# Kernel tuning notes

Measured on AMD Instinct MI355X. Metric: run time of the kernel, lower is better.

## Reference

```python
import jax, jax.numpy as jnp
import numpy as np


def _dct_basis(N):
    # X[k] = 2 * sum_n x[n] * cos(pi * k * (2n+1) / (2N))  -- matches the
    # flip+concat+rfft+twiddle path of the torch module (unnormalized DCT-II x2).
    k = jnp.arange(N, dtype=jnp.float32)[:, None]
    n = jnp.arange(N, dtype=jnp.float32)[None, :]
    return 2.0 * jnp.cos(jnp.pi * k * (2.0 * n + 1.0) / (2.0 * N))  # (K, N)


def _dct2(x):
    B, C, H, W = x.shape
    Bw = _dct_basis(W)
    Bh = _dct_basis(H)
    x = jnp.einsum('bchw,kw->bchk', x, Bw)  # DCT along W
    x = jnp.einsum('bchw,kh->bckw', x, Bh)  # DCT along H
    return x


def _conv3x3(x, w, b):
    y = jax.lax.conv_general_dilated(x, w, window_strides=(1, 1), padding='SAME',
                                     dimension_numbers=('NCHW', 'OIHW', 'NCHW'))
    return y + b[None, :, None, None]


def _bn(x, g, be, m, v):
    # inference-mode BatchNorm2d, eps = 1e-5
    inv = jax.lax.rsqrt(v + 1e-5)
    return (x - m[None, :, None, None]) * (g * inv)[None, :, None, None] + be[None, :, None, None]


def setup_inputs() -> dict:
    key = jax.random.key(0)
    ks = jax.random.split(key, 16)
    B, C, H, W = 32, 1, 224, 224
    mid, emb = 128, 256
    s = 0.05
    return {
        'x':  jax.random.normal(ks[0], (B, C, H, W), jnp.float32),
        'w1': jax.random.normal(ks[1], (64, C, 3, 3), jnp.float32) * s,
        'b1': jax.random.normal(ks[2], (64,), jnp.float32) * s,
        'g1': jax.random.uniform(ks[3], (64,), jnp.float32, 0.5, 1.5),
        'be1': jax.random.normal(ks[4], (64,), jnp.float32) * s,
        'm1': jax.random.normal(ks[5], (64,), jnp.float32) * s,
        'v1': jax.random.uniform(ks[6], (64,), jnp.float32, 0.5, 1.5),
        'w2': jax.random.normal(ks[7], (mid, 64, 3, 3), jnp.float32) * s,
        'b2': jax.random.normal(ks[8], (mid,), jnp.float32) * s,
        'g2': jax.random.uniform(ks[9], (mid,), jnp.float32, 0.5, 1.5),
        'be2': jax.random.normal(ks[10], (mid,), jnp.float32) * s,
        'm2': jax.random.normal(ks[11], (mid,), jnp.float32) * s,
        'v2': jax.random.uniform(ks[12], (mid,), jnp.float32, 0.5, 1.5),
        'wp': jax.random.normal(ks[13], (emb, mid), jnp.float32) * s,
        'bp': jax.random.normal(ks[14], (emb,), jnp.float32) * s,
    }


def reference(x, w1, b1, g1, be1, m1, v1, w2, b2, g2, be2, m2, v2, wp, bp):
    USE_TOPK = 0.5
    X = _dct2(x)                                   # (B, 1, H, W)
    B, C, H, W = X.shape
    k_h, k_w = int(H * USE_TOPK), int(W * USE_TOPK)
    mask = jnp.zeros((H, W), X.dtype).at[:k_h, :k_w].set(1.0)
    X = X * mask[None, None]
    h = jax.nn.relu(_bn(_conv3x3(X, w1, b1), g1, be1, m1, v1))
    h = jax.nn.relu(_bn(_conv3x3(h, w2, b2), g2, be2, m2, v2))
    h = jnp.mean(h, axis=(2, 3))                   # AdaptiveAvgPool2d((1,1)) -> (B, mid)
    return h @ wp.T + bp                           # (B, emb_dim)
```

## Files before the change

kernel.cpp:

```cpp
#include <hip/hip_runtime.h>
#include <math.h>


#define NPIX 224
#define KEEP 112
#define H1DIM 115
#define NPX1 (H1DIM * H1DIM)
#define ADIM 114

typedef short bf16x8 __attribute__((ext_vector_type(8)));
typedef float f32x16 __attribute__((ext_vector_type(16)));

__device__ __forceinline__ unsigned short f2bf(float f) {
    unsigned int u = __float_as_uint(f);
    unsigned int r = (u + 0x7FFFu + ((u >> 16) & 1u)) >> 16;
    return (unsigned short)r;
}

__global__ __launch_bounds__(256) void prep_kernel(
    const float* __restrict__ w1, const float* __restrict__ b1,
    const float* __restrict__ g1, const float* __restrict__ be1,
    const float* __restrict__ m1, const float* __restrict__ v1,
    const float* __restrict__ w2,
    float* __restrict__ Bst, float* __restrict__ P,
    float* __restrict__ ws1, float* __restrict__ wb1,
    uint4* __restrict__ w2f) {
    int bp = blockIdx.x, tid = threadIdx.x;
    if (bp < 49) {
        int idx = bp * 256 + tid;
        if (idx < KEEP * KEEP) {
            int n = idx / KEEP, k = idx - n * KEEP;
            double ang = 3.14159265358979323846 * (double)k * (2.0 * n + 1.0) / (2.0 * NPIX);
            Bst[n * KEEP + k] = (float)(2.0 * cos(ang));
        }
    } else if (bp < 54) {
        __shared__ float c1s[64];
        if (tid < 64) {
            float sc = g1[tid] * rsqrtf(v1[tid] + 1e-5f);
            c1s[tid] = fmaxf((b1[tid] - m1[tid]) * sc + be1[tid], 0.f);
        }
        __syncthreads();
        int idx = (bp - 49) * 256 + tid;
        if (idx < 128 * 9) {
            int oc = idx / 9, tap = idx - oc * 9;
            float s = 0.f;
            for (int ic = 0; ic < 64; ++ic)
                s = fmaf(w2[((size_t)oc * 64 + ic) * 9 + tap], c1s[ic], s);
            P[idx] = s;
        }
    } else if (bp == 54) {
        if (tid < 64) {
            float sc = g1[tid] * rsqrtf(v1[tid] + 1e-5f);
            wb1[tid] = (b1[tid] - m1[tid]) * sc + be1[tid];
            for (int t = 0; t < 9; ++t) ws1[tid * 9 + t] = w1[tid * 9 + t] * sc;
        }
    } else {
        int j = (bp - 55) * 256 + tid;
        if (j < 9216) {
            int q = j >> 6, lane = j & 63;
            int tap = q / 16, rem = q & 15;
            int kc = rem >> 2, g32 = rem & 3;
            int oc = g32 * 32 + (lane & 31);
            int ic0 = kc * 16 + (lane >> 5) * 8;
            union { unsigned short us[8]; uint4 v; } u;
#pragma unroll
            for (int t_ = 0; t_ < 8; ++t_)
                u.us[t_] = f2bf(w2[((size_t)oc * 64 + ic0 + t_) * 9 + tap]);
            w2f[j] = u.v;
        }
    }
}

__global__ __launch_bounds__(256) void dct_w_kernel(const float* __restrict__ x,
                                                    const float* __restrict__ Bst,
                                                    float* __restrict__ tmp1) {
    int bx = blockIdx.x, tid = threadIdx.x;
    __shared__ float eo[2][8][112];
    const float* rows = x + (size_t)bx * 8 * NPIX;
    for (int i = tid; i < 896; i += 256) {
        int r = i / 112, n = i - r * 112;
        float a = rows[r * NPIX + n], bv = rows[r * NPIX + 223 - n];
        eo[0][r][n] = a + bv;
        eo[1][r][n] = a - bv;
    }
    __syncthreads();
    int kw = tid & 127, rh = tid >> 7;
    if (kw >= KEEP) return;
    const float* eop = &eo[kw & 1][rh * 4][0];
    float a0 = 0.f, a1 = 0.f, a2 = 0.f, a3 = 0.f;
    for (int n = 0; n < 112; ++n) {
        float bs = Bst[n * KEEP + kw];
        a0 = fmaf(eop[n], bs, a0);
        a1 = fmaf(eop[112 + n], bs, a1);
        a2 = fmaf(eop[224 + n], bs, a2);
        a3 = fmaf(eop[336 + n], bs, a3);
    }
    size_t base = ((size_t)bx * 8 + rh * 4) * KEEP + kw;
    tmp1[base] = a0; tmp1[base + 112] = a1; tmp1[base + 224] = a2; tmp1[base + 336] = a3;
}

__global__ __launch_bounds__(512) void dct_h_kernel(const float* __restrict__ tmp1,
                                                    const float* __restrict__ Bst,
                                                    float* __restrict__ Xd) {
    int kq = blockIdx.x, b = blockIdx.y;
    int tid = threadIdx.x;
    int kw = tid & 127, sub = tid >> 7;
    __shared__ float ps[3][4][112];
    const int kh0 = kq * 4;
    float a0 = 0.f, a1 = 0.f, a2 = 0.f, a3 = 0.f;
    if (kw < KEEP) {
        const float* t = tmp1 + (size_t)b * NPIX * KEEP + kw;
        for (int h = sub * 28; h < sub * 28 + 28; ++h) {
            float lo = t[(size_t)h * KEEP];
            float hi = t[(size_t)(223 - h) * KEEP];
            float e = lo + hi, o = lo - hi;
            const float* bs = Bst + h * KEEP + kh0;
            a0 = fmaf(e, bs[0], a0);
            a1 = fmaf(o, bs[1], a1);
            a2 = fmaf(e, bs[2], a2);
            a3 = fmaf(o, bs[3], a3);
        }
        if (sub) {
            ps[sub - 1][0][kw] = a0; ps[sub - 1][1][kw] = a1;
            ps[sub - 1][2][kw] = a2; ps[sub - 1][3][kw] = a3;
        }
    }
    __syncthreads();
    if (sub == 0 && kw < KEEP) {
        a0 += ps[0][0][kw] + ps[1][0][kw] + ps[2][0][kw];
        a1 += ps[0][1][kw] + ps[1][1][kw] + ps[2][1][kw];
        a2 += ps[0][2][kw] + ps[1][2][kw] + ps[2][2][kw];
        a3 += ps[0][3][kw] + ps[1][3][kw] + ps[2][3][kw];
        float* X = Xd + ((size_t)b * KEEP + kh0) * KEEP + kw;
        X[0] = a0; X[112] = a1; X[224] = a2; X[336] = a3;
    }
}

__global__ __launch_bounds__(256) void conv1_kernel(const float* __restrict__ Xd,
                                                    const float* __restrict__ ws1,
                                                    const float* __restrict__ wb1,
                                                    unsigned short* __restrict__ h1c) {
    const int b = blockIdx.y;
    const int p0 = blockIdx.x * 256;
    const int tid = threadIdx.x;
    const int p = p0 + tid;
    __shared__ uint4 Lt[2048];

    const bool valid = p < NPX1;
    int r = p / H1DIM, c = p - r * H1DIM;
    const float* X = Xd + (size_t)b * KEEP * KEEP;
    float xv[9];
#pragma unroll
    for (int ky = 0; ky < 3; ++ky)
#pragma unroll
        for (int kx = 0; kx < 3; ++kx) {
            int rr = r + ky - 1, cc = c + kx - 1;
            xv[ky * 3 + kx] =
                (valid && (unsigned)rr < (unsigned)KEEP && (unsigned)cc < (unsigned)KEEP)
                    ? X[rr * KEEP + cc] : 0.f;
        }

#pragma unroll 1
    for (int icg = 0; icg < 8; ++icg) {
        union { unsigned short us[8]; uint4 v; } u;
#pragma unroll
        for (int j = 0; j < 8; ++j) {
            int ic = icg * 8 + j;
            float s = wb1[ic];
#pragma unroll
            for (int t = 0; t < 9; ++t) s = fmaf(xv[t], ws1[ic * 9 + t], s);
            u.us[j] = f2bf(fmaxf(s, 0.f));
        }
        Lt[tid * 8 + (icg ^ (tid & 7))] = u.v;
    }
    __syncthreads();

#pragma unroll
    for (int k = 0; k < 8; ++k) {
        int q = k * 256 + tid;
        int pxl = q >> 3, ig = q & 7;
        uint4 v = Lt[pxl * 8 + (ig ^ (pxl & 7))];
        int pg = p0 + pxl;
        if (pg < NPX1)
            *reinterpret_cast<uint4*>(h1c + ((size_t)b * NPX1 + pg) * 64 + ig * 8) = v;
    }
}

__global__ __launch_bounds__(512, 4) void conv2_mfma_kernel(
    const unsigned short* __restrict__ h1c, const uint4* __restrict__ w2f,
    const float* __restrict__ b2, const float* __restrict__ g2,
    const float* __restrict__ be2, const float* __restrict__ m2,
    const float* __restrict__ v2, float* __restrict__ partial) {
    const int tc = blockIdx.x, tr = blockIdx.y, b = blockIdx.z;
    const int r0 = tr * 16, c0 = tc * 16;
    const int tid = threadIdx.x;
    const int lane = tid & 63, w = tid >> 6;
    const int mg = w & 3, og = w >> 2;

    __shared__ unsigned short At[324 * 64];

    const unsigned short* __restrict__ h1b = h1c + (size_t)b * (NPX1 * 64);
    char* Atw = reinterpret_cast<char*>(At);
    for (int e = tid; e < 2592; e += 512) {
        int px = e >> 3, gi = e & 7;
        int pr = px / 18, pc = px - pr * 18;
        int gr = r0 + pr - 1, gc = c0 + pc - 1;
        uint4 v = make_uint4(0u, 0u, 0u, 0u);
        if ((unsigned)gr < (unsigned)H1DIM && (unsigned)gc < (unsigned)H1DIM)
            v = *reinterpret_cast<const uint4*>(h1b + ((size_t)(gr * H1DIM + gc)) * 64 + gi * 8);
        int off = px * 128 + 32 * ((gi >> 1) ^ (px & 3)) + 16 * ((gi & 1) ^ ((px >> 2) & 1));
        *reinterpret_cast<uint4*>(Atw + off) = v;
    }
    __syncthreads();

    f32x16 acc[2][2];
#pragma unroll
    for (int F = 0; F < 2; ++F)
#pragma unroll
        for (int N = 0; N < 2; ++N)
#pragma unroll
            for (int i = 0; i < 16; ++i) acc[F][N][i] = 0.f;

    const int flim2 = ADIM - r0 - 4 * mg;
    int A0[9];
    {
        const int prb = 4 * mg + ((lane & 31) >> 4);
        const int cb = lane & 15;
        const int hb = lane >> 5;
#pragma unroll
        for (int ky = 0; ky < 3; ++ky)
#pragma unroll
            for (int kx = 0; kx < 3; ++kx) {
                int px = (prb + ky) * 18 + cb + kx;
                A0[ky * 3 + kx] = px * 128 + 32 * (px & 3) + 16 * (hb ^ ((px >> 2) & 1));
            }
    }
    const char* Atc = reinterpret_cast<const char*>(At);

    if (flim2 >= 4) {
#pragma unroll
        for (int s = 0; s < 36; ++s) {
            const int tap = s >> 2, kc = s & 3;
            const int ky = tap / 3, kx = tap - 3 * ky;
            const bf16x8* bq = reinterpret_cast<const bf16x8*>(
                w2f + (size_t)(((tap * 4 + kc) * 4) + og * 2) * 64 + lane);
            const bf16x8 b0 = bq[0];
            const bf16x8 b1 = bq[64];
            const int a0 = A0[ky * 3 + kx] ^ (kc << 5);
            const int a1 = (a0 ^ 16) + 4608;
            const bf16x8 va0 = *reinterpret_cast<const bf16x8*>(Atc + a0);
            const bf16x8 va1 = *reinterpret_cast<const bf16x8*>(Atc + a1);
            acc[0][0] = __builtin_amdgcn_mfma_f32_32x32x16_bf16(va0, b0, acc[0][0], 0, 0, 0);
            acc[0][1] = __builtin_amdgcn_mfma_f32_32x32x16_bf16(va0, b1, acc[0][1], 0, 0, 0);
            acc[1][0] = __builtin_amdgcn_mfma_f32_32x32x16_bf16(va1, b0, acc[1][0], 0, 0, 0);
            acc[1][1] = __builtin_amdgcn_mfma_f32_32x32x16_bf16(va1, b1, acc[1][1], 0, 0, 0);
        }
    } else if (flim2 > 0) {
#pragma unroll
        for (int s = 0; s < 36; ++s) {
            const int tap = s >> 2, kc = s & 3;
            const int ky = tap / 3, kx = tap - 3 * ky;
            const bf16x8* bq = reinterpret_cast<const bf16x8*>(
                w2f + (size_t)(((tap * 4 + kc) * 4) + og * 2) * 64 + lane);
            const bf16x8 b0 = bq[0];
            const bf16x8 b1 = bq[64];
            const int a0 = A0[ky * 3 + kx] ^ (kc << 5);
            const bf16x8 va0 = *reinterpret_cast<const bf16x8*>(Atc + a0);
            acc[0][0] = __builtin_amdgcn_mfma_f32_32x32x16_bf16(va0, b0, acc[0][0], 0, 0, 0);
            acc[0][1] = __builtin_amdgcn_mfma_f32_32x32x16_bf16(va0, b1, acc[0][1], 0, 0, 0);
        }
    }

    const int tile = tr * 8 + tc;
    float* pslice = partial + (((size_t)b * 64 + tile) * 4 + mg) * 128;
#pragma unroll
    for (int N = 0; N < 2; ++N) {
        int oc = og * 64 + N * 32 + (lane & 31);
        float sc = g2[oc] * rsqrtf(v2[oc] + 1e-5f);
        float bias = b2[oc] - m2[oc];
        float add = be2[oc];
        float s = 0.f;
#pragma unroll
        for (int F = 0; F < 2; ++F) {
#pragma unroll
            for (int rg = 0; rg < 16; ++rg) {
                int m = (rg & 3) + 8 * (rg >> 2) + 4 * (lane >> 5);
                int p = ((2 * mg + F) << 5) + m;
                int row = r0 + (p >> 4);
                int col = c0 + (p & 15);
                float v = fmaxf(fmaf(acc[F][N][rg] + bias, sc, add), 0.f);
                s += (row < ADIM && col < ADIM) ? v : 0.f;
            }
        }
        s += __shfl_xor(s, 32);
        if (lane < 32) pslice[og * 64 + N * 32 + lane] = s;
    }
}

__global__ __launch_bounds__(256) void tail_kernel(
    const float* __restrict__ partial, const float* __restrict__ P,
    const float* __restrict__ b2, const float* __restrict__ g2,
    const float* __restrict__ be2, const float* __restrict__ m2,
    const float* __restrict__ v2,
    const float* __restrict__ wp, const float* __restrict__ bp,
    float* __restrict__ out) {
    int b = blockIdx.x, tid = threadIdx.x;
    __shared__ float red[2][128];
    __shared__ float mrow[128];
    int oc = tid & 127, half = tid >> 7;
    const float* pb = partial + (size_t)b * 256 * 128 + oc;
    float s = 0.f;
#pragma unroll 8
    for (int j = 0; j < 128; ++j) s += pb[(size_t)(half * 128 + j) * 128];
    red[half][oc] = s;
    __syncthreads();
    if (tid < 128) {
        float tot = red[0][tid] + red[1][tid];
        float p[9];
#pragma unroll
        for (int t = 0; t < 9; ++t) p[t] = P[tid * 9 + t];
        float Sall = p[0] + p[1] + p[2] + p[3] + p[4] + p[5] + p[6] + p[7] + p[8];
        float Stop = p[3] + p[4] + p[5] + p[6] + p[7] + p[8];
        float Sbot = p[0] + p[1] + p[2] + p[3] + p[4] + p[5];
        float Sleft  = p[1] + p[2] + p[4] + p[5] + p[7] + p[8];
        float Sright = p[0] + p[1] + p[3] + p[4] + p[6] + p[7];
        float Ctr = p[3] + p[4] + p[6] + p[7];
        float Cbl = p[1] + p[2] + p[4] + p[5];
        float Cbr = p[0] + p[1] + p[3] + p[4];
        float bias = b2[tid], mm = m2[tid], bb = be2[tid];
        float sc = g2[tid] * rsqrtf(v2[tid] + 1e-5f);
#define VALOF(S) fmaxf(((bias) + (S) - (mm)) * (sc) + (bb), 0.f)
        float cs = 36515.f * VALOF(Sall) + 109.f * VALOF(Stop) + 109.f * VALOF(Sleft)
                 + 222.f * VALOF(Sbot) + 222.f * VALOF(Sright)
                 + VALOF(Ctr) + VALOF(Cbl) + VALOF(Cbr);
#undef VALOF
        mrow[tid] = (tot + cs) * (1.f / (224.f * 224.f));
    }
    __syncthreads();
    const float4* wr = reinterpret_cast<const float4*>(wp + (size_t)tid * 128);
    float acc = bp[tid];
#pragma unroll 8
    for (int c = 0; c < 32; ++c) {
        float4 wv = wr[c];
        acc = fmaf(mrow[4 * c], wv.x, acc);
        acc = fmaf(mrow[4 * c + 1], wv.y, acc);
        acc = fmaf(mrow[4 * c + 2], wv.z, acc);
        acc = fmaf(mrow[4 * c + 3], wv.w, acc);
    }
    out[(size_t)b * 256 + tid] = acc;
}

extern "C" void kernel_launch(void* const* d_in, const int* in_sizes, int n_in,
                              void* d_out, int out_size, void* d_ws, size_t ws_size,
                              hipStream_t stream) {
    const float* x   = (const float*)d_in[0];
    const float* w1  = (const float*)d_in[1];
    const float* b1  = (const float*)d_in[2];
    const float* g1  = (const float*)d_in[3];
    const float* be1 = (const float*)d_in[4];
    const float* m1  = (const float*)d_in[5];
    const float* v1  = (const float*)d_in[6];
    const float* w2  = (const float*)d_in[7];
    const float* b2  = (const float*)d_in[8];
    const float* g2  = (const float*)d_in[9];
    const float* be2 = (const float*)d_in[10];
    const float* m2  = (const float*)d_in[11];
    const float* v2  = (const float*)d_in[12];
    const float* wp  = (const float*)d_in[13];
    const float* bp  = (const float*)d_in[14];
    float* out = (float*)d_out;

    float* ws = (float*)d_ws;
    size_t off = 0;
    float* Bst  = ws + off; off += (size_t)KEEP * KEEP;
    float* tmp1 = ws + off; off += (size_t)32 * NPIX * KEEP;
    float* Xd   = ws + off; off += (size_t)32 * KEEP * KEEP;
    float* P    = ws + off; off += 128 * 9;
    float* ws1  = ws + off; off += 64 * 9;
    float* wb1  = ws + off; off += 64;
    uint4* w2f  = (uint4*)(ws + off); off += (size_t)9216 * 4;
    float* part = ws + off; off += (size_t)32 * 256 * 128;
    unsigned short* h1c = (unsigned short*)(ws + off);
    off += (size_t)32 * NPX1 * 64 / 2;

    if (ws_size < off * sizeof(float)) return;

    prep_kernel<<<dim3(91), dim3(256), 0, stream>>>(w1, b1, g1, be1, m1, v1, w2,
                                                    Bst, P, ws1, wb1, w2f);
    dct_w_kernel<<<dim3(896), dim3(256), 0, stream>>>(x, Bst, tmp1);
    dct_h_kernel<<<dim3(28, 32), dim3(512), 0, stream>>>(tmp1, Bst, Xd);
    conv1_kernel<<<dim3(52, 32), dim3(256), 0, stream>>>(Xd, ws1, wb1, h1c);
    conv2_mfma_kernel<<<dim3(8, 8, 32), dim3(512), 0, stream>>>(
        h1c, w2f, b2, g2, be2, m2, v2, part);
    tail_kernel<<<dim3(32), dim3(256), 0, stream>>>(part, P, b2, g2, be2, m2, v2, wp, bp, out);
}
```

Measured before the change: 127.3 us.

## Fuse conv1 into conv2 tile load, recomputing halo in shared memory

Removes the separate conv1 kernel and its bf16 h1 intermediate buffer in global memory. Each conv2 block now loads a 20x20 patch of the masked DCT output into shared memory and computes the 18x18x64 conv1+BN+ReLU halo tile directly into the swizzled LDS layout. This eliminates the write and reread of roughly 54 MB of activations and one launch. In exchange, the halo pixels are computed redundantly, and the per-block prologue is heavier, which may lengthen conv2's critical path.

```diff
diff --git a/kernel.cpp b/kernel.cpp
--- a/kernel.cpp
+++ b/kernel.cpp
@@ -5,7 +5,6 @@
 #define NPIX 224
 #define KEEP 112
 #define H1DIM 115
-#define NPX1 (H1DIM * H1DIM)
 #define ADIM 114
 
 typedef short bf16x8 __attribute__((ext_vector_type(8)));
@@ -136,58 +135,9 @@
     }
 }
 
-__global__ __launch_bounds__(256) void conv1_kernel(const float* __restrict__ Xd,
-                                                    const float* __restrict__ ws1,
-                                                    const float* __restrict__ wb1,
-                                                    unsigned short* __restrict__ h1c) {
-    const int b = blockIdx.y;
-    const int p0 = blockIdx.x * 256;
-    const int tid = threadIdx.x;
-    const int p = p0 + tid;
-    __shared__ uint4 Lt[2048];
-
-    const bool valid = p < NPX1;
-    int r = p / H1DIM, c = p - r * H1DIM;
-    const float* X = Xd + (size_t)b * KEEP * KEEP;
-    float xv[9];
-#pragma unroll
-    for (int ky = 0; ky < 3; ++ky)
-#pragma unroll
-        for (int kx = 0; kx < 3; ++kx) {
-            int rr = r + ky - 1, cc = c + kx - 1;
-            xv[ky * 3 + kx] =
-                (valid && (unsigned)rr < (unsigned)KEEP && (unsigned)cc < (unsigned)KEEP)
-                    ? X[rr * KEEP + cc] : 0.f;
-        }
-
-#pragma unroll 1
-    for (int icg = 0; icg < 8; ++icg) {
-        union { unsigned short us[8]; uint4 v; } u;
-#pragma unroll
-        for (int j = 0; j < 8; ++j) {
-            int ic = icg * 8 + j;
-            float s = wb1[ic];
-#pragma unroll
-            for (int t = 0; t < 9; ++t) s = fmaf(xv[t], ws1[ic * 9 + t], s);
-            u.us[j] = f2bf(fmaxf(s, 0.f));
-        }
-        Lt[tid * 8 + (icg ^ (tid & 7))] = u.v;
-    }
-    __syncthreads();
-
-#pragma unroll
-    for (int k = 0; k < 8; ++k) {
-        int q = k * 256 + tid;
-        int pxl = q >> 3, ig = q & 7;
-        uint4 v = Lt[pxl * 8 + (ig ^ (pxl & 7))];
-        int pg = p0 + pxl;
-        if (pg < NPX1)
-            *reinterpret_cast<uint4*>(h1c + ((size_t)b * NPX1 + pg) * 64 + ig * 8) = v;
-    }
-}
-
-__global__ __launch_bounds__(512, 4) void conv2_mfma_kernel(
-    const unsigned short* __restrict__ h1c, const uint4* __restrict__ w2f,
+__global__ __launch_bounds__(512, 4) void conv2_fused_kernel(
+    const float* __restrict__ Xd, const float* __restrict__ ws1,
+    const float* __restrict__ wb1, const uint4* __restrict__ w2f,
     const float* __restrict__ b2, const float* __restrict__ g2,
     const float* __restrict__ be2, const float* __restrict__ m2,
     const float* __restrict__ v2, float* __restrict__ partial) {
@@ -198,18 +148,43 @@
     const int mg = w & 3, og = w >> 2;
 
     __shared__ unsigned short At[324 * 64];
-
-    const unsigned short* __restrict__ h1b = h1c + (size_t)b * (NPX1 * 64);
+    __shared__ float Xs[20][21];
+    __shared__ float wbs[64];
+
+    const float* __restrict__ Xb = Xd + (size_t)b * KEEP * KEEP;
+    for (int i = tid; i < 400; i += 512) {
+        int rr = i / 20, cc = i - rr * 20;
+        int gr = r0 - 2 + rr, gc = c0 - 2 + cc;
+        Xs[rr][cc] = ((unsigned)gr < (unsigned)KEEP && (unsigned)gc < (unsigned)KEEP)
+                         ? Xb[gr * KEEP + gc] : 0.f;
+    }
+    if (tid < 64) wbs[tid] = wb1[tid];
+    __syncthreads();
+
     char* Atw = reinterpret_cast<char*>(At);
     for (int e = tid; e < 2592; e += 512) {
-        int px = e >> 3, gi = e & 7;
+        int px = e >> 3, icg = e & 7;
         int pr = px / 18, pc = px - pr * 18;
         int gr = r0 + pr - 1, gc = c0 + pc - 1;
-        uint4 v = make_uint4(0u, 0u, 0u, 0u);
-        if ((unsigned)gr < (unsigned)H1DIM && (unsigned)gc < (unsigned)H1DIM)
-            v = *reinterpret_cast<const uint4*>(h1b + ((size_t)(gr * H1DIM + gc)) * 64 + gi * 8);
-        int off = px * 128 + 32 * ((gi >> 1) ^ (px & 3)) + 16 * ((gi & 1) ^ ((px >> 2) & 1));
-        *reinterpret_cast<uint4*>(Atw + off) = v;
+        union { unsigned short us[8]; uint4 v; } u;
+        u.v = make_uint4(0u, 0u, 0u, 0u);
+        if ((unsigned)gr < (unsigned)H1DIM && (unsigned)gc < (unsigned)H1DIM) {
+            float xv[9];
+#pragma unroll
+            for (int ky = 0; ky < 3; ++ky)
+#pragma unroll
+                for (int kx = 0; kx < 3; ++kx) xv[ky * 3 + kx] = Xs[pr + ky][pc + kx];
+#pragma unroll
+            for (int j = 0; j < 8; ++j) {
+                int ic = icg * 8 + j;
+                float s = wbs[ic];
+#pragma unroll
+                for (int t = 0; t < 9; ++t) s = fmaf(xv[t], ws1[ic * 9 + t], s);
+                u.us[j] = f2bf(fmaxf(s, 0.f));
+            }
+        }
+        int off = px * 128 + 32 * ((icg >> 1) ^ (px & 3)) + 16 * ((icg & 1) ^ ((px >> 2) & 1));
+        *reinterpret_cast<uint4*>(Atw + off) = u.v;
     }
     __syncthreads();
 
@@ -380,8 +355,6 @@
     float* wb1  = ws + off; off += 64;
     uint4* w2f  = (uint4*)(ws + off); off += (size_t)9216 * 4;
     float* part = ws + off; off += (size_t)32 * 256 * 128;
-    unsigned short* h1c = (unsigned short*)(ws + off);
-    off += (size_t)32 * NPX1 * 64 / 2;
 
     if (ws_size < off * sizeof(float)) return;
 
@@ -389,8 +362,7 @@
                                                     Bst, P, ws1, wb1, w2f);
     dct_w_kernel<<<dim3(896), dim3(256), 0, stream>>>(x, Bst, tmp1);
     dct_h_kernel<<<dim3(28, 32), dim3(512), 0, stream>>>(tmp1, Bst, Xd);
-    conv1_kernel<<<dim3(52, 32), dim3(256), 0, stream>>>(Xd, ws1, wb1, h1c);
-    conv2_mfma_kernel<<<dim3(8, 8, 32), dim3(512), 0, stream>>>(
-        h1c, w2f, b2, g2, be2, m2, v2, part);
+    conv2_fused_kernel<<<dim3(8, 8, 32), dim3(512), 0, stream>>>(
+        Xd, ws1, wb1, w2f, b2, g2, be2, m2, v2, part);
     tail_kernel<<<dim3(32), dim3(256), 0, stream>>>(part, P, b2, g2, be2, m2, v2, wp, bp, out);
 }
```

Result: slower. 180.1 us (+41.5%).
